# Kernel optimization log

Hardware: AMD Instinct MI355X
Metric: run time of the kernel (lower is better)

Reference implementation:

```python
import jax, jax.numpy as jnp
import numpy as np
import math

N_HEAD = 8
N_FEAT = 512
D_K = N_FEAT // N_HEAD
B, T = 4, 2048


def setup_inputs() -> dict:
    key = jax.random.key(0)
    ks = jax.random.split(key, 16)
    s = 1.0 / math.sqrt(N_FEAT)
    return {
        "x": jax.random.normal(ks[0], (B, T, N_FEAT), dtype=jnp.float32),
        "pos_emb": jax.random.normal(ks[1], (1, T, N_FEAT), dtype=jnp.float32),
        "Wq": jax.random.normal(ks[2], (N_FEAT, N_FEAT), dtype=jnp.float32) * s,
        "bq": jnp.zeros((N_FEAT,), dtype=jnp.float32),
        "Wk": jax.random.normal(ks[3], (N_FEAT, N_FEAT), dtype=jnp.float32) * s,
        "bk": jnp.zeros((N_FEAT,), dtype=jnp.float32),
        "Wv": jax.random.normal(ks[4], (N_FEAT, N_FEAT), dtype=jnp.float32) * s,
        "bv": jnp.zeros((N_FEAT,), dtype=jnp.float32),
        "Wpos": jax.random.normal(ks[5], (N_FEAT, N_FEAT), dtype=jnp.float32) * s,
        "Wout": jax.random.normal(ks[6], (N_FEAT, N_FEAT), dtype=jnp.float32) * s,
        "bout": jnp.zeros((N_FEAT,), dtype=jnp.float32),
        "pos_bias_u": jax.random.normal(ks[7], (N_HEAD, D_K), dtype=jnp.float32) * 0.05,
        "pos_bias_v": jax.random.normal(ks[8], (N_HEAD, D_K), dtype=jnp.float32) * 0.05,
    }


def reference(x, pos_emb, Wq, bq, Wk, bk, Wv, bv, Wpos, Wout, bout,
              pos_bias_u, pos_bias_v):
    b, t, f = x.shape
    h, d = N_HEAD, D_K
    # QKV projections (torch Linear: y = x @ W.T + b), split into heads -> (B,H,T,d)
    q = (jnp.einsum('btf,of->bto', x, Wq) + bq).reshape(b, t, h, d).transpose(0, 2, 1, 3)
    k = (jnp.einsum('btf,of->bto', x, Wk) + bk).reshape(b, t, h, d).transpose(0, 2, 1, 3)
    v = (jnp.einsum('btf,of->bto', x, Wv) + bv).reshape(b, t, h, d).transpose(0, 2, 1, 3)
    # positional projection: (1, T_pos, F) -> (H, T_pos, d)
    tp = pos_emb.shape[1]
    p = jnp.einsum('ptf,of->pto', pos_emb, Wpos).reshape(tp, h, d).transpose(1, 0, 2)
    q_u = q + pos_bias_u[None, :, None, :]  # (B,H,T,d)
    q_v = q + pos_bias_v[None, :, None, :]
    matrix_ac = jnp.einsum('bhtd,bhsd->bhts', q_u, k)   # content-content
    matrix_bd = jnp.einsum('bhtd,hsd->bhts', q_v, p)    # content-position
    scores = (matrix_ac + matrix_bd) / math.sqrt(d)
    attn = jax.nn.softmax(scores, axis=-1)  # dropout is identity in eval mode
    out = jnp.einsum('bhts,bhsd->bhtd', attn, v)
    out = out.transpose(0, 2, 1, 3).reshape(b, t, h * d)
    return jnp.einsum('btf,of->bto', out, Wout) + bout
```

## Files before the change

kernel.cpp:

```cpp
#include <hip/hip_runtime.h>

typedef float f4 __attribute__((ext_vector_type(4)));
typedef __attribute__((ext_vector_type(8))) short bf16x8;
typedef __attribute__((ext_vector_type(4))) float f32x4;

#define T_SEQ 2048
#define NFEAT 512
#define NHEAD 8
#define DK    64
#define BATCH 4

using gptr_t = const __attribute__((address_space(1))) void*;
using lptr_t = __attribute__((address_space(3))) void*;

static __device__ __forceinline__ short f2bf(float f) {
    unsigned u = __builtin_bit_cast(unsigned, f);
    u += 0x7fff + ((u >> 16) & 1);
    return (short)(u >> 16);
}
static __device__ __forceinline__ float b2f(short s) {
    unsigned u = ((unsigned)(unsigned short)s) << 16;
    return __builtin_bit_cast(float, u);
}

__global__ __launch_bounds__(256) void cvt_kernel(
    const float* __restrict__ x, const float* __restrict__ pos,
    const float* __restrict__ Wq, const float* __restrict__ Wk, const float* __restrict__ Wv,
    const float* __restrict__ Wpos, const float* __restrict__ Wout,
    const float* __restrict__ bq, const float* __restrict__ bk, const float* __restrict__ bv,
    short* __restrict__ xb, short* __restrict__ posb, short* __restrict__ wqkv,
    short* __restrict__ wpb, short* __restrict__ wob, float* __restrict__ bqkv)
{
    const int blk = blockIdx.x;
    const float* src; short* dst; int off;
    if      (blk < 2048) { src = x;    dst = xb;          off = blk * 2048; }
    else if (blk < 2560) { src = pos;  dst = posb;        off = (blk - 2048) * 2048; }
    else if (blk < 2688) { src = Wq;   dst = wqkv;        off = (blk - 2560) * 2048; }
    else if (blk < 2816) { src = Wk;   dst = wqkv + 262144; off = (blk - 2688) * 2048; }
    else if (blk < 2944) { src = Wv;   dst = wqkv + 524288; off = (blk - 2816) * 2048; }
    else if (blk < 3072) { src = Wpos; dst = wpb;         off = (blk - 2944) * 2048; }
    else if (blk < 3200) { src = Wout; dst = wob;         off = (blk - 3072) * 2048; }
    else {
        int t = threadIdx.x;
        bqkv[t]        = bq[t];        bqkv[256 + t]  = bq[256 + t];
        bqkv[512 + t]  = bk[t];        bqkv[768 + t]  = bk[256 + t];
        bqkv[1024 + t] = bv[t];        bqkv[1280 + t] = bv[256 + t];
        return;
    }
    int i = off + threadIdx.x * 8;
    f4 a = *(const f4*)(src + i);
    f4 b = *(const f4*)(src + i + 4);
    bf16x8 o;
#pragma unroll
    for (int j = 0; j < 4; ++j) { o[j] = f2bf(a[j]); o[4 + j] = f2bf(b[j]); }
    *(bf16x8*)(dst + i) = o;
}

template<int OUT_BF16>
static __device__ __forceinline__ void gemm_tile(
    short* As, short* Bs,
    const short* __restrict__ A, const short* __restrict__ B,
    const float* __restrict__ bias, void* __restrict__ Cv,
    int N, int K, int row0, int col0)
{
    const int tid = threadIdx.x, lane = tid & 63, wave = tid >> 6;
    const int col = lane & 15, quad = lane >> 4;
    const int wm = (wave >> 1) * 64, wn = (wave & 1) * 64;
    const int rl = lane & 15;

    const short* Abase = A + (size_t)(row0 + wave * 32 + rl) * K + (lane >> 4) * 8;
    const short* Bbase = B + (size_t)(col0 + wave * 32 + rl) * K + (lane >> 4) * 8;

    f32x4 acc[4][4];
#pragma unroll
    for (int i = 0; i < 4; ++i)
#pragma unroll
        for (int j = 0; j < 4; ++j) acc[i][j] = (f32x4){0.f, 0.f, 0.f, 0.f};

    for (int k0 = 0; k0 < K; k0 += 64) {
        __syncthreads();
#pragma unroll
        for (int c = 0; c < 2; ++c)
#pragma unroll
            for (int hf = 0; hf < 2; ++hf) {
                __builtin_amdgcn_global_load_lds((gptr_t)(Abase + (size_t)(16 * c) * K + k0 + hf * 32),
                                                 (lptr_t)(As + wave * 2048 + c * 1024 + hf * 512), 16, 0, 0);
                __builtin_amdgcn_global_load_lds((gptr_t)(Bbase + (size_t)(16 * c) * K + k0 + hf * 32),
                                                 (lptr_t)(Bs + wave * 2048 + c * 1024 + hf * 512), 16, 0, 0);
            }
        __syncthreads();
#pragma unroll
        for (int kt = 0; kt < 2; ++kt) {
            bf16x8 af[4], bfr[4];
#pragma unroll
            for (int mt = 0; mt < 4; ++mt)
                af[mt] = *(const bf16x8*)&As[((wm >> 4) + mt) * 1024 + (kt * 4 + quad) * 128 + col * 8];
#pragma unroll
            for (int nt = 0; nt < 4; ++nt)
                bfr[nt] = *(const bf16x8*)&Bs[((wn >> 4) + nt) * 1024 + (kt * 4 + quad) * 128 + col * 8];
#pragma unroll
            for (int mt = 0; mt < 4; ++mt)
#pragma unroll
                for (int nt = 0; nt < 4; ++nt)
                    acc[mt][nt] = __builtin_amdgcn_mfma_f32_16x16x32_bf16(af[mt], bfr[nt], acc[mt][nt], 0, 0, 0);
        }
    }

    float bv4[4];
#pragma unroll
    for (int nt = 0; nt < 4; ++nt)
        bv4[nt] = bias ? bias[col0 + wn + nt * 16 + col] : 0.f;
#pragma unroll
    for (int mt = 0; mt < 4; ++mt)
#pragma unroll
        for (int reg = 0; reg < 4; ++reg) {
            int r = row0 + wm + mt * 16 + quad * 4 + reg;
#pragma unroll
            for (int nt = 0; nt < 4; ++nt) {
                int c = col0 + wn + nt * 16 + col;
                float v = acc[mt][nt][reg] + bv4[nt];
                if (OUT_BF16) ((short*)Cv)[(size_t)r * N + c] = f2bf(v);
                else          ((float*)Cv)[(size_t)r * N + c] = v;
            }
        }
}

__global__ __launch_bounds__(256) void gemm_qkv_pos(
    const short* __restrict__ xb, const short* __restrict__ wqkv,
    const float* __restrict__ bqkv, short* __restrict__ QKV,
    const short* __restrict__ posb, const short* __restrict__ wpb,
    short* __restrict__ Pm)
{
    __shared__ short As[8192], Bs[8192];
    const int bid = blockIdx.x;
    if (bid < 768) {
        gemm_tile<1>(As, Bs, xb, wqkv, bqkv, QKV, 1536, 512, (bid / 12) * 128, (bid % 12) * 128);
    } else {
        const int t = bid - 768;
        gemm_tile<1>(As, Bs, posb, wpb, nullptr, Pm, 512, 512, (t / 4) * 128, (t % 4) * 128);
    }
}

__global__ __launch_bounds__(256) void gemm_out_kernel(
    const short* __restrict__ A, const short* __restrict__ B,
    const float* __restrict__ bias, float* __restrict__ C)
{
    __shared__ short As[8192], Bs[8192];
    gemm_tile<0>(As, Bs, A, B, bias, C, 512, 512, blockIdx.y * 128, blockIdx.x * 128);
}

__global__ __launch_bounds__(256) void kvprep_kernel(
    const short* __restrict__ qkv, const short* __restrict__ pm,
    const float* __restrict__ u, const float* __restrict__ vb,
    short* __restrict__ kp, short* __restrict__ vt, float* __restrict__ cb)
{
    __shared__ short tile[64][72];
    const int tid = threadIdx.x, lr = tid >> 2, lc = (tid & 3) * 16;
    const int bh = blockIdx.y, b = bh >> 3, h = bh & 7, s0 = blockIdx.x * 64;

    const short* kptr = qkv + (size_t)(b * T_SEQ + s0 + lr) * 1536 + 512 + h * DK + lc;
    const short* pptr = pm + (size_t)(s0 + lr) * NFEAT + h * DK + lc;
    const short* vptr = qkv + (size_t)(b * T_SEQ + s0 + lr) * 1536 + 1024 + h * DK + lc;
    bf16x8 k0_ = *(const bf16x8*)kptr,       k1_ = *(const bf16x8*)(kptr + 8);
    bf16x8 p0_ = *(const bf16x8*)pptr,       p1_ = *(const bf16x8*)(pptr + 8);
    bf16x8 v0_ = *(const bf16x8*)vptr,       v1_ = *(const bf16x8*)(vptr + 8);

    float c = 0.f;
    bf16x8 o0, o1;
#pragma unroll
    for (int j = 0; j < 8; ++j) {
        float kf = b2f(k0_[j]), pf = b2f(p0_[j]);
        o0[j] = f2bf(kf + pf);
        c += u[h * DK + lc + j] * kf + vb[h * DK + lc + j] * pf;
        float kf1 = b2f(k1_[j]), pf1 = b2f(p1_[j]);
        o1[j] = f2bf(kf1 + pf1);
        c += u[h * DK + lc + 8 + j] * kf1 + vb[h * DK + lc + 8 + j] * pf1;
    }
    short* kpd = kp + ((size_t)bh * T_SEQ + s0 + lr) * DK + lc;
    *(bf16x8*)kpd       = o0;
    *(bf16x8*)(kpd + 8) = o1;
    c += __shfl_xor(c, 1);
    c += __shfl_xor(c, 2);
    if ((tid & 3) == 0) cb[(size_t)bh * T_SEQ + s0 + lr] = 0.125f * c;

    *(bf16x8*)&tile[lr][lc]     = v0_;
    *(bf16x8*)&tile[lr][lc + 8] = v1_;
    __syncthreads();
    short* dst = vt + (size_t)(bh * DK + lr) * T_SEQ + s0 + lc;
    bf16x8 t0_, t1_;
#pragma unroll
    for (int j = 0; j < 8; ++j) { t0_[j] = tile[lc + j][lr]; t1_[j] = tile[lc + 8 + j][lr]; }
    *(bf16x8*)dst       = t0_;
    *(bf16x8*)(dst + 8) = t1_;
}

__global__ __launch_bounds__(512) void attn_kernel(
    const short* __restrict__ qkv, const short* __restrict__ kp,
    const short* __restrict__ vt, const float* __restrict__ cb,
    short* __restrict__ attO)
{
    __shared__ __align__(16) short Qs[128][72], KPs[64][72], Vts[64][72], Ps[8][16][72];
    __shared__ float cs[64];
    const int tid = threadIdx.x, lane = tid & 63, wave = tid >> 6;
    const int col = lane & 15, quad = lane >> 4;
    const int bh = blockIdx.y, b = bh >> 3, h = bh & 7, t0 = blockIdx.x * 128;

    {
        const int lr = tid >> 2, lc = (tid & 3) * 16;
        const short* qp = qkv + (size_t)(b * T_SEQ + t0 + lr) * 1536 + h * DK + lc;
        *(bf16x8*)&Qs[lr][lc]     = *(const bf16x8*)qp;
        *(bf16x8*)&Qs[lr][lc + 8] = *(const bf16x8*)(qp + 8);
    }
    const int lr8 = tid >> 3, lc8 = (tid & 7) * 8;

    f32x4 Oacc[4];
    float lsum[4] = {0.f, 0.f, 0.f, 0.f};
#pragma unroll
    for (int i = 0; i < 4; ++i) Oacc[i] = (f32x4){0.f, 0.f, 0.f, 0.f};

    for (int s0 = 0; s0 < T_SEQ; s0 += 64) {
        __syncthreads();
        *(bf16x8*)&KPs[lr8][lc8] = *(const bf16x8*)(kp + ((size_t)bh * T_SEQ + s0 + lr8) * DK + lc8);
        *(bf16x8*)&Vts[lr8][lc8] = *(const bf16x8*)(vt + (size_t)(bh * DK + lr8) * T_SEQ + s0 + lc8);
        if (tid < 64) cs[tid] = cb[(size_t)bh * T_SEQ + s0 + tid];
        __syncthreads();

        f32x4 S[4];
#pragma unroll
        for (int nt = 0; nt < 4; ++nt) S[nt] = (f32x4){0.f, 0.f, 0.f, 0.f};
#pragma unroll
        for (int kt = 0; kt < 2; ++kt) {
            bf16x8 a = *(const bf16x8*)&Qs[wave * 16 + col][kt * 32 + quad * 8];
#pragma unroll
            for (int nt = 0; nt < 4; ++nt) {
                bf16x8 bb = *(const bf16x8*)&KPs[nt * 16 + col][kt * 32 + quad * 8];
                S[nt] = __builtin_amdgcn_mfma_f32_16x16x32_bf16(a, bb, S[nt], 0, 0, 0);
            }
        }
        float c0 = cs[col], c1 = cs[16 + col], c2 = cs[32 + col], c3 = cs[48 + col];
#pragma unroll
        for (int reg = 0; reg < 4; ++reg) {
            int r = quad * 4 + reg;
            float e0 = __expf(fmaf(S[0][reg], 0.125f, c0));
            float e1 = __expf(fmaf(S[1][reg], 0.125f, c1));
            float e2 = __expf(fmaf(S[2][reg], 0.125f, c2));
            float e3 = __expf(fmaf(S[3][reg], 0.125f, c3));
            lsum[reg] += (e0 + e1) + (e2 + e3);
            Ps[wave][r][col]      = f2bf(e0);
            Ps[wave][r][16 + col] = f2bf(e1);
            Ps[wave][r][32 + col] = f2bf(e2);
            Ps[wave][r][48 + col] = f2bf(e3);
        }
        __syncthreads();
#pragma unroll
        for (int kt = 0; kt < 2; ++kt) {
            bf16x8 pa = *(const bf16x8*)&Ps[wave][col][kt * 32 + quad * 8];
#pragma unroll
            for (int dt = 0; dt < 4; ++dt) {
                bf16x8 vb = *(const bf16x8*)&Vts[dt * 16 + col][kt * 32 + quad * 8];
                Oacc[dt] = __builtin_amdgcn_mfma_f32_16x16x32_bf16(pa, vb, Oacc[dt], 0, 0, 0);
            }
        }
    }
#pragma unroll
    for (int reg = 0; reg < 4; ++reg) {
        float l = lsum[reg];
#pragma unroll
        for (int off = 1; off < 16; off <<= 1) l += __shfl_xor(l, off);
        float inv = 1.f / l;
        int t = t0 + wave * 16 + quad * 4 + reg;
        short* op = attO + (size_t)(b * T_SEQ + t) * NFEAT + h * DK;
#pragma unroll
        for (int dt = 0; dt < 4; ++dt)
            op[dt * 16 + col] = f2bf(Oacc[dt][reg] * inv);
    }
}

extern "C" void kernel_launch(void* const* d_in, const int* in_sizes, int n_in,
                              void* d_out, int out_size, void* d_ws, size_t ws_size,
                              hipStream_t stream)
{
    const float* x    = (const float*)d_in[0];
    const float* pos  = (const float*)d_in[1];
    const float* Wq   = (const float*)d_in[2];
    const float* bq   = (const float*)d_in[3];
    const float* Wk   = (const float*)d_in[4];
    const float* bk   = (const float*)d_in[5];
    const float* Wv   = (const float*)d_in[6];
    const float* bv   = (const float*)d_in[7];
    const float* Wpos = (const float*)d_in[8];
    const float* Wout = (const float*)d_in[9];
    const float* bout = (const float*)d_in[10];
    const float* pbu  = (const float*)d_in[11];
    const float* pbv  = (const float*)d_in[12];
    float* out = (float*)d_out;

    short* xb   = (short*)d_ws;
    short* posb = xb   + 4194304;
    short* wqkv = posb + 1048576;
    short* wpb  = wqkv + 786432;
    short* wob  = wpb  + 262144;
    short* QKV  = wob  + 262144;
    short* Pm   = QKV  + 12582912;
    short* KP   = Pm   + 1048576;
    short* Vt   = KP   + 4194304;
    short* AttO = Vt   + 4194304;
    float* bqkv = (float*)(AttO + 4194304);
    float* Cb   = bqkv + 1536;

    cvt_kernel<<<dim3(3201), dim3(256), 0, stream>>>(x, pos, Wq, Wk, Wv, Wpos, Wout, bq, bk, bv,
                                                     xb, posb, wqkv, wpb, wob, bqkv);
    gemm_qkv_pos<<<dim3(832), dim3(256), 0, stream>>>(xb, wqkv, bqkv, QKV, posb, wpb, Pm);
    kvprep_kernel<<<dim3(T_SEQ / 64, BATCH * NHEAD), dim3(256), 0, stream>>>(QKV, Pm, pbu, pbv, KP, Vt, Cb);
    attn_kernel<<<dim3(T_SEQ / 128, BATCH * NHEAD), dim3(512), 0, stream>>>(QKV, KP, Vt, Cb, AttO);
    gemm_out_kernel<<<dim3(512 / 128, 8192 / 128), dim3(256), 0, stream>>>(AttO, wob, bout, out);
}
```

Baseline: 236.0 us.

## Prefetch K/V tiles into registers, use exp2, remap blocks for XCD locality

The attention kernel now loads the next K/V/bias tile into registers while the current tile is computed, and keeps Q fragments in registers instead of reloading them from LDS every step. The softmax uses exp2 with log2(e) folded into the scale and bias, switches to a cheaper round-half-up bf16 conversion, and removes the barrier between writing P and the PV matmul, since each wave only reads its own slice of P. Block indices in the attention kernel and both GEMMs are remapped so that blocks sharing inputs land on the same XCD, which is meant to improve L2 reuse. In exchange there is higher register pressure, a slightly different rounding, and a wasted wraparound prefetch on the last step.

```diff
diff --git a/kernel.cpp b/kernel.cpp
--- a/kernel.cpp
+++ b/kernel.cpp
@@ -13,10 +13,16 @@
 using gptr_t = const __attribute__((address_space(1))) void*;
 using lptr_t = __attribute__((address_space(3))) void*;
 
+#define LOG2E_8 0.18033688011f
+
 static __device__ __forceinline__ short f2bf(float f) {
     unsigned u = __builtin_bit_cast(unsigned, f);
     u += 0x7fff + ((u >> 16) & 1);
     return (short)(u >> 16);
+}
+static __device__ __forceinline__ short f2bfr(float f) {
+    unsigned u = __builtin_bit_cast(unsigned, f);
+    return (short)((u + 0x8000u) >> 16);
 }
 static __device__ __forceinline__ float b2f(short s) {
     unsigned u = ((unsigned)(unsigned short)s) << 16;
@@ -134,7 +140,9 @@
     __shared__ short As[8192], Bs[8192];
     const int bid = blockIdx.x;
     if (bid < 768) {
-        gemm_tile<1>(As, Bs, xb, wqkv, bqkv, QKV, 1536, 512, (bid / 12) * 128, (bid % 12) * 128);
+        const int xcd = bid & 7, s = bid >> 3;
+        const int row = xcd * 8 + (s & 7), colt = s >> 3;
+        gemm_tile<1>(As, Bs, xb, wqkv, bqkv, QKV, 1536, 512, row * 128, colt * 128);
     } else {
         const int t = bid - 768;
         gemm_tile<1>(As, Bs, posb, wpb, nullptr, Pm, 512, 512, (t / 4) * 128, (t % 4) * 128);
@@ -146,7 +154,10 @@
     const float* __restrict__ bias, float* __restrict__ C)
 {
     __shared__ short As[8192], Bs[8192];
-    gemm_tile<0>(As, Bs, A, B, bias, C, 512, 512, blockIdx.y * 128, blockIdx.x * 128);
+    const int bid = blockIdx.x;
+    const int xcd = bid & 7, s = bid >> 3;
+    const int row = xcd * 8 + (s & 7), colt = s >> 3;
+    gemm_tile<0>(As, Bs, A, B, bias, C, 512, 512, row * 128, colt * 128);
 }
 
 __global__ __launch_bounds__(256) void kvprep_kernel(
@@ -181,7 +192,7 @@
     *(bf16x8*)(kpd + 8) = o1;
     c += __shfl_xor(c, 1);
     c += __shfl_xor(c, 2);
-    if ((tid & 3) == 0) cb[(size_t)bh * T_SEQ + s0 + lr] = 0.125f * c;
+    if ((tid & 3) == 0) cb[(size_t)bh * T_SEQ + s0 + lr] = LOG2E_8 * c;
 
     *(bf16x8*)&tile[lr][lc]     = v0_;
     *(bf16x8*)&tile[lr][lc + 8] = v1_;
@@ -203,7 +214,11 @@
     __shared__ float cs[64];
     const int tid = threadIdx.x, lane = tid & 63, wave = tid >> 6;
     const int col = lane & 15, quad = lane >> 4;
-    const int bh = blockIdx.y, b = bh >> 3, h = bh & 7, t0 = blockIdx.x * 128;
+    const int idx = blockIdx.x;
+    const int xcd = idx & 7, slot = idx >> 3;
+    const int bh = (slot >> 4) * 8 + xcd;
+    const int t0 = (slot & 15) * 128;
+    const int b = bh >> 3, h = bh & 7;
 
     {
         const int lr = tid >> 2, lc = (tid & 3) * 16;
@@ -213,6 +228,14 @@
     }
     const int lr8 = tid >> 3, lc8 = (tid & 7) * 8;
 
+    bf16x8 kpr = *(const bf16x8*)(kp + ((size_t)bh * T_SEQ + lr8) * DK + lc8);
+    bf16x8 vtr = *(const bf16x8*)(vt + ((size_t)(bh * DK + lr8)) * T_SEQ + lc8);
+    float cbr = (tid < 64) ? cb[(size_t)bh * T_SEQ + tid] : 0.f;
+
+    __syncthreads();
+    bf16x8 qa0 = *(const bf16x8*)&Qs[wave * 16 + col][quad * 8];
+    bf16x8 qa1 = *(const bf16x8*)&Qs[wave * 16 + col][32 + quad * 8];
+
     f32x4 Oacc[4];
     float lsum[4] = {0.f, 0.f, 0.f, 0.f};
 #pragma unroll
@@ -220,38 +243,40 @@
 
     for (int s0 = 0; s0 < T_SEQ; s0 += 64) {
         __syncthreads();
-        *(bf16x8*)&KPs[lr8][lc8] = *(const bf16x8*)(kp + ((size_t)bh * T_SEQ + s0 + lr8) * DK + lc8);
-        *(bf16x8*)&Vts[lr8][lc8] = *(const bf16x8*)(vt + (size_t)(bh * DK + lr8) * T_SEQ + s0 + lc8);
-        if (tid < 64) cs[tid] = cb[(size_t)bh * T_SEQ + s0 + tid];
+        *(bf16x8*)&KPs[lr8][lc8] = kpr;
+        *(bf16x8*)&Vts[lr8][lc8] = vtr;
+        if (tid < 64) cs[tid] = cbr;
         __syncthreads();
 
+        const int sn = (s0 + 64) & (T_SEQ - 1);
+        kpr = *(const bf16x8*)(kp + ((size_t)bh * T_SEQ + sn + lr8) * DK + lc8);
+        vtr = *(const bf16x8*)(vt + ((size_t)(bh * DK + lr8)) * T_SEQ + sn + lc8);
+        if (tid < 64) cbr = cb[(size_t)bh * T_SEQ + sn + tid];
+
         f32x4 S[4];
 #pragma unroll
         for (int nt = 0; nt < 4; ++nt) S[nt] = (f32x4){0.f, 0.f, 0.f, 0.f};
 #pragma unroll
-        for (int kt = 0; kt < 2; ++kt) {
-            bf16x8 a = *(const bf16x8*)&Qs[wave * 16 + col][kt * 32 + quad * 8];
-#pragma unroll
-            for (int nt = 0; nt < 4; ++nt) {
-                bf16x8 bb = *(const bf16x8*)&KPs[nt * 16 + col][kt * 32 + quad * 8];
-                S[nt] = __builtin_amdgcn_mfma_f32_16x16x32_bf16(a, bb, S[nt], 0, 0, 0);
-            }
-        }
-        float c0 = cs[col], c1 = cs[16 + col], c2 = cs[32 + col], c3 = cs[48 + col];
+        for (int nt = 0; nt < 4; ++nt) {
+            bf16x8 b0 = *(const bf16x8*)&KPs[nt * 16 + col][quad * 8];
+            S[nt] = __builtin_amdgcn_mfma_f32_16x16x32_bf16(qa0, b0, S[nt], 0, 0, 0);
+            bf16x8 b1 = *(const bf16x8*)&KPs[nt * 16 + col][32 + quad * 8];
+            S[nt] = __builtin_amdgcn_mfma_f32_16x16x32_bf16(qa1, b1, S[nt], 0, 0, 0);
+        }
+        const float c0 = cs[col], c1 = cs[16 + col], c2 = cs[32 + col], c3 = cs[48 + col];
 #pragma unroll
         for (int reg = 0; reg < 4; ++reg) {
             int r = quad * 4 + reg;
-            float e0 = __expf(fmaf(S[0][reg], 0.125f, c0));
-            float e1 = __expf(fmaf(S[1][reg], 0.125f, c1));
-            float e2 = __expf(fmaf(S[2][reg], 0.125f, c2));
-            float e3 = __expf(fmaf(S[3][reg], 0.125f, c3));
+            float e0 = __builtin_amdgcn_exp2f(fmaf(S[0][reg], LOG2E_8, c0));
+            float e1 = __builtin_amdgcn_exp2f(fmaf(S[1][reg], LOG2E_8, c1));
+            float e2 = __builtin_amdgcn_exp2f(fmaf(S[2][reg], LOG2E_8, c2));
+            float e3 = __builtin_amdgcn_exp2f(fmaf(S[3][reg], LOG2E_8, c3));
             lsum[reg] += (e0 + e1) + (e2 + e3);
-            Ps[wave][r][col]      = f2bf(e0);
-            Ps[wave][r][16 + col] = f2bf(e1);
-            Ps[wave][r][32 + col] = f2bf(e2);
-            Ps[wave][r][48 + col] = f2bf(e3);
-        }
-        __syncthreads();
+            Ps[wave][r][col]      = f2bfr(e0);
+            Ps[wave][r][16 + col] = f2bfr(e1);
+            Ps[wave][r][32 + col] = f2bfr(e2);
+            Ps[wave][r][48 + col] = f2bfr(e3);
+        }
 #pragma unroll
         for (int kt = 0; kt < 2; ++kt) {
             bf16x8 pa = *(const bf16x8*)&Ps[wave][col][kt * 32 + quad * 8];
@@ -312,6 +337,6 @@
                                                      xb, posb, wqkv, wpb, wob, bqkv);
     gemm_qkv_pos<<<dim3(832), dim3(256), 0, stream>>>(xb, wqkv, bqkv, QKV, posb, wpb, Pm);
     kvprep_kernel<<<dim3(T_SEQ / 64, BATCH * NHEAD), dim3(256), 0, stream>>>(QKV, Pm, pbu, pbv, KP, Vt, Cb);
-    attn_kernel<<<dim3(T_SEQ / 128, BATCH * NHEAD), dim3(512), 0, stream>>>(QKV, KP, Vt, Cb, AttO);
-    gemm_out_kernel<<<dim3(512 / 128, 8192 / 128), dim3(256), 0, stream>>>(AttO, wob, bout, out);
-}
+    attn_kernel<<<dim3(512), dim3(512), 0, stream>>>(QKV, KP, Vt, Cb, AttO);
+    gemm_out_kernel<<<dim3(256), dim3(256), 0, stream>>>(AttO, wob, bout, out);
+}
```

Measured after the change: 215.3 us. 8.8% less time.
